# Kernel optimization log

Hardware: AMD Instinct MI355X
Metric: run time of the kernel (lower is better)

The kernel has to match this reference:

```python
import jax, jax.numpy as jnp
import numpy as np

PATCH = 14
LEVELS = 6
DIM = 512
MULT = 4
ITERS = 12
TOKEN_ATTEND_SELF_VALUE = -0.0005


def _grouped_ff(x, w1, b1, w2, b2):
    # x: [b, n, g, d]; per-group 1x1 conv == per-level MLP
    h = jnp.einsum('bnld,lmd->bnlm', x, w1) + b1  # [b,n,g,d*mult]
    h = jax.nn.gelu(h, approximate=False)
    return jnp.einsum('bnlm,ldm->bnld', h, w2) + b2


def _consensus(levels):
    # levels: [b, n, l, d]
    d = levels.shape[-1]
    n = levels.shape[1]
    k = levels / jnp.maximum(jnp.linalg.norm(levels, axis=-1, keepdims=True), 1e-12)
    sim = jnp.einsum('bild,bjld->blij', levels, k) * (d ** -0.5)
    self_mask = jnp.eye(n, dtype=bool)[None, None]  # attend_self=False
    sim = jnp.where(self_mask, TOKEN_ATTEND_SELF_VALUE, sim)
    attn = jax.nn.softmax(sim, axis=-1)
    return jnp.einsum('blij,bjld->bild', attn, levels)


def setup_inputs() -> dict:
    key = jax.random.key(0)
    ks = jax.random.split(key, 12)
    b, c, hw = 16, 1, 224
    pd = PATCH * PATCH * c  # 196
    nps = hw // PATCH
    n = nps * nps  # 256
    s = 0.02
    return {
        'img': jax.random.normal(ks[0], (b, c, hw, hw), jnp.float32),
        'to_tokens_w': jax.random.normal(ks[1], (pd, DIM), jnp.float32) * s,
        'to_tokens_b': jnp.zeros((DIM,), jnp.float32),
        'pos_emb': jax.random.normal(ks[2], (n, DIM), jnp.float32) * s,
        'init_levels': jax.random.normal(ks[3], (LEVELS, DIM), jnp.float32),
        'bu_w1': jax.random.normal(ks[4], (LEVELS, DIM * MULT, DIM), jnp.float32) * s,
        'bu_b1': jnp.zeros((LEVELS, DIM * MULT), jnp.float32),
        'bu_w2': jax.random.normal(ks[5], (LEVELS, DIM, DIM * MULT), jnp.float32) * s,
        'bu_b2': jnp.zeros((LEVELS, DIM), jnp.float32),
        'td_w1': jax.random.normal(ks[6], (LEVELS - 1, DIM * MULT, DIM), jnp.float32) * s,
        'td_b1': jnp.zeros((LEVELS - 1, DIM * MULT), jnp.float32),
        'td_w2': jax.random.normal(ks[7], (LEVELS - 1, DIM, DIM * MULT), jnp.float32) * s,
        'td_b2': jnp.zeros((LEVELS - 1, DIM), jnp.float32),
    }


def reference(img, to_tokens_w, to_tokens_b, pos_emb, init_levels,
              bu_w1, bu_b1, bu_w2, bu_b2, td_w1, td_b1, td_w2, td_b2):
    b, c, H, W = img.shape
    hp, wp = H // PATCH, W // PATCH
    n = hp * wp
    # b c (hp p1) (wp p2) -> b (hp wp) (p1 p2 c)
    x = img.reshape(b, c, hp, PATCH, wp, PATCH)
    x = x.transpose(0, 2, 4, 3, 5, 1).reshape(b, n, PATCH * PATCH * c)
    tokens = x @ to_tokens_w + to_tokens_b          # [b, n, d]
    pos = pos_emb[None, :, None, :]                 # [1, n, 1, d]
    bottom = tokens[:, :, None, :]                  # [b, n, 1, d]
    levels0 = jnp.broadcast_to(init_levels[None, None], (b, n, LEVELS, DIM))
    contrib = jnp.array([4., 4., 4., 4., 4., 3.], jnp.float32)[None, None, :, None]

    def step(levels, _):
        lwi = jnp.concatenate((bottom, levels), axis=2)         # [b, n, L+1, d]
        bu = _grouped_ff(lwi[:, :, :-1], bu_w1, bu_b1, bu_w2, bu_b2)
        td = _grouped_ff(lwi[:, :, 2:] + pos, td_w1, td_b1, td_w2, td_b2)
        td = jnp.pad(td, ((0, 0), (0, 0), (0, 1), (0, 0)))      # zero pad top level
        cons = _consensus(levels)
        new_levels = (levels + bu + td + cons) / contrib
        return new_levels, None

    levels, _ = jax.lax.scan(step, levels0, None, length=ITERS)
    return levels
```

## Files before the change

### kernel.cpp

```cpp
#include <hip/hip_runtime.h>
#include <hip/hip_bf16.h>
#include <math.h>

typedef unsigned short ushort_t;

#define DEV __device__ __forceinline__

DEV float bf2f(ushort_t u) {
  return __uint_as_float(((unsigned int)u) << 16);
}
DEV ushort_t f2bf(float f) {
  unsigned int x = __float_as_uint(f);
  return (ushort_t)((x + 0x7FFFu + ((x >> 16) & 1u)) >> 16);
}

DEV float gelu_f(float x) {
  float z = fabsf(x) * 0.70710678118654752f;
  float t = __builtin_amdgcn_rcpf(1.0f + 0.3275911f * z);
  float p = t * (0.254829592f +
            t * (-0.284496736f +
            t * (1.421413741f +
            t * (-1.453152027f +
            t * 1.061405429f))));
  float e = 1.0f - p * __expf(-z * z);
  float s = (x >= 0.f) ? e : -e;
  return 0.5f * x * (1.0f + s);
}

using bf16x8 = __attribute__((ext_vector_type(8))) __bf16;
using f32x4  = __attribute__((ext_vector_type(4))) float;

DEV void gload16(const ushort_t* g, ushort_t* l) {
  __builtin_amdgcn_global_load_lds((const __attribute__((address_space(1))) void*)g,
                                   (__attribute__((address_space(3))) void*)l, 16, 0, 0);
}

DEV void stage_sw(const ushort_t* g, int ld, ushort_t* lds, int t) {
  int w = t >> 6;
#pragma unroll
  for (int r = 0; r < 4; ++r) {
    int chunk = r * 256 + t;
    int row = chunk >> 3;
    int sw  = ((chunk & 7) ^ (row & 7)) * 8;
    const ushort_t* gp = g + (size_t)row * ld + sw;
    ushort_t* lp = lds + (size_t)(r * 256 + w * 64) * 8;
    gload16(gp, lp);
  }
}

template <typename F>
DEV void gemm_tile(const ushort_t* A, int lda, const ushort_t* B, int ldb, int K, F&& epi) {
  __shared__ alignas(16) ushort_t As[2][128 * 64];
  __shared__ alignas(16) ushort_t Bs[2][128 * 64];
  int t = threadIdx.x;
  int lane = t & 63;
  int w = t >> 6;
  int wr = w >> 1, wc = w & 1;
  const int nk = K >> 6;
  f32x4 acc[4][4];
#pragma unroll
  for (int m = 0; m < 4; ++m)
#pragma unroll
    for (int n = 0; n < 4; ++n) acc[m][n] = (f32x4){0.f, 0.f, 0.f, 0.f};

  int aoff[4][2], boff[4][2];
#pragma unroll
  for (int m = 0; m < 4; ++m)
#pragma unroll
    for (int kk = 0; kk < 2; ++kk) {
      int ks = kk * 4 + (lane >> 4);
      aoff[m][kk] = (wr * 64 + m * 16 + (lane & 15)) * 64 + ((ks ^ (lane & 7)) * 8);
      boff[m][kk] = (wc * 64 + m * 16 + (lane & 15)) * 64 + ((ks ^ (lane & 7)) * 8);
    }

  stage_sw(A, lda, As[0], t);
  stage_sw(B, ldb, Bs[0], t);

  for (int kt = 0; kt < nk; ++kt) {
    int cur = kt & 1;
    int nxt = (kt + 1 < nk) ? kt + 1 : kt;
    stage_sw(A + (size_t)nxt * 64, lda, As[cur ^ 1], t);
    stage_sw(B + (size_t)nxt * 64, ldb, Bs[cur ^ 1], t);
    asm volatile("s_waitcnt vmcnt(8)" ::: "memory");
    __builtin_amdgcn_s_barrier();
    __builtin_amdgcn_sched_barrier(0);
    const ushort_t* asb = &As[cur][0];
    const ushort_t* bsb = &Bs[cur][0];
#pragma unroll
    for (int kk = 0; kk < 2; ++kk) {
      bf16x8 af[4], bfr[4];
#pragma unroll
      for (int m = 0; m < 4; ++m) af[m] = *(const bf16x8*)&asb[aoff[m][kk]];
#pragma unroll
      for (int n = 0; n < 4; ++n) bfr[n] = *(const bf16x8*)&bsb[boff[n][kk]];
      __builtin_amdgcn_s_setprio(1);
#pragma unroll
      for (int m = 0; m < 4; ++m)
#pragma unroll
        for (int n = 0; n < 4; ++n)
          acc[m][n] = __builtin_amdgcn_mfma_f32_16x16x32_bf16(af[m], bfr[n], acc[m][n], 0, 0, 0);
      __builtin_amdgcn_s_setprio(0);
    }
    __builtin_amdgcn_s_barrier();
  }

#pragma unroll
  for (int m = 0; m < 4; ++m)
#pragma unroll
    for (int n = 0; n < 4; ++n)
#pragma unroll
      for (int r = 0; r < 4; ++r) {
        int lr = wr * 64 + m * 16 + (lane >> 4) * 4 + r;
        int lc = wc * 64 + n * 16 + (lane & 15);
        epi(lr, lc, acc[m][n][r]);
      }
}

#define MFMA_QUAD(QM, QN)                                                      \
  _Pragma("unroll") for (int m_ = 0; m_ < 4; ++m_)                             \
  _Pragma("unroll") for (int n_ = 0; n_ < 2; ++n_)                             \
  _Pragma("unroll") for (int kk_ = 0; kk_ < 2; ++kk_)                          \
    acc[QM][QN][m_][n_] = __builtin_amdgcn_mfma_f32_16x16x32_bf16(             \
        aF[m_][kk_], bF[QN][n_][kk_], acc[QM][QN][m_][n_], 0, 0, 0);

template <typename F>
DEV void gemm256(const ushort_t* A, int lda, const ushort_t* B, int ldb, int K, F&& epi) {
  __shared__ alignas(16) ushort_t As[2][256 * 64];
  __shared__ alignas(16) ushort_t Bs[2][256 * 64];
  const int tid = threadIdx.x;
  const int lane = tid & 63;
  const int w = tid >> 6;
  const int ur = w >> 2, uc = w & 3;
  const int nk = K >> 6;

  const int c0 = tid, c1 = 512 + tid;
  const int row0 = c0 >> 3, row1 = c1 >> 3;
  const int sw0 = ((c0 & 7) ^ (row0 & 7)) * 8;
  const int sw1 = ((c1 & 7) ^ (row1 & 7)) * 8;
  const ushort_t* Ab0 = A + (size_t)row0 * lda + sw0;
  const ushort_t* Ab1 = A + (size_t)row1 * lda + sw1;
  const ushort_t* Bb0 = B + (size_t)row0 * ldb + sw0;
  const ushort_t* Bb1 = B + (size_t)row1 * ldb + sw1;
  const int ld0 = (0 * 512 + w * 64) * 8;
  const int ld1 = (1 * 512 + w * 64) * 8;

  auto stageA = [&](int t, int hh, int b) {
    const ushort_t* g0 = Ab0 + (size_t)hh * 128 * lda + t * 64;
    const ushort_t* g1 = Ab1 + (size_t)hh * 128 * lda + t * 64;
    ushort_t* l = &As[b][hh * 8192];
    gload16(g0, l + ld0);
    gload16(g1, l + ld1);
  };
  auto stageB = [&](int t, int hh, int b) {
    const ushort_t* g0 = Bb0 + (size_t)hh * 128 * ldb + t * 64;
    const ushort_t* g1 = Bb1 + (size_t)hh * 128 * ldb + t * 64;
    ushort_t* l = &Bs[b][hh * 8192];
    gload16(g0, l + ld0);
    gload16(g1, l + ld1);
  };

  int aoff[4][2], boff[2][2];
#pragma unroll
  for (int m = 0; m < 4; ++m)
#pragma unroll
    for (int kk = 0; kk < 2; ++kk) {
      int row = ur * 64 + m * 16 + (lane & 15);
      int ks = kk * 4 + (lane >> 4);
      aoff[m][kk] = row * 64 + ((ks ^ (lane & 7)) * 8);
    }
#pragma unroll
  for (int n = 0; n < 2; ++n)
#pragma unroll
    for (int kk = 0; kk < 2; ++kk) {
      int row = uc * 32 + n * 16 + (lane & 15);
      int ks = kk * 4 + (lane >> 4);
      boff[n][kk] = row * 64 + ((ks ^ (lane & 7)) * 8);
    }

  f32x4 acc[2][2][4][2];
#pragma unroll
  for (int qm = 0; qm < 2; ++qm)
#pragma unroll
    for (int qn = 0; qn < 2; ++qn)
#pragma unroll
      for (int m = 0; m < 4; ++m)
#pragma unroll
        for (int n = 0; n < 2; ++n) acc[qm][qn][m][n] = (f32x4){0.f, 0.f, 0.f, 0.f};

  stageA(0, 0, 0);
  stageB(0, 0, 0);
  stageB(0, 1, 0);
  stageA(0, 1, 0);
  stageA(1, 0, 1);
  stageB(1, 0, 1);
  asm volatile("s_waitcnt vmcnt(8)" ::: "memory");
  __builtin_amdgcn_s_barrier();

  bf16x8 aF[4][2], bF[2][2][2];

  for (int t = 0; t < nk; ++t) {
    const int b = t & 1;
    const ushort_t* asb = &As[b][0];
    const ushort_t* bsb = &Bs[b][0];
    const int t1 = (t + 1 < nk) ? t + 1 : nk - 1;
    const int t2 = (t + 2 < nk) ? t + 2 : nk - 1;

#pragma unroll
    for (int m = 0; m < 4; ++m)
#pragma unroll
      for (int kk = 0; kk < 2; ++kk) aF[m][kk] = *(const bf16x8*)&asb[aoff[m][kk]];
#pragma unroll
    for (int n = 0; n < 2; ++n)
#pragma unroll
      for (int kk = 0; kk < 2; ++kk) bF[0][n][kk] = *(const bf16x8*)&bsb[boff[n][kk]];
    stageB(t1, 1, (t + 1) & 1);
    __builtin_amdgcn_s_barrier();
    asm volatile("s_waitcnt lgkmcnt(0)" ::: "memory");
    __builtin_amdgcn_s_setprio(1);
    MFMA_QUAD(0, 0)
    __builtin_amdgcn_s_setprio(0);
    asm volatile("s_waitcnt vmcnt(8)" ::: "memory");
    __builtin_amdgcn_s_barrier();

#pragma unroll
    for (int n = 0; n < 2; ++n)
#pragma unroll
      for (int kk = 0; kk < 2; ++kk) bF[1][n][kk] = *(const bf16x8*)&bsb[boff[n][kk] + 8192];
    stageA(t1, 1, (t + 1) & 1);
    __builtin_amdgcn_s_barrier();
    asm volatile("s_waitcnt lgkmcnt(0)" ::: "memory");
    __builtin_amdgcn_s_setprio(1);
    MFMA_QUAD(0, 1)
    __builtin_amdgcn_s_setprio(0);
    asm volatile("s_waitcnt vmcnt(8)" ::: "memory");
    __builtin_amdgcn_s_barrier();

#pragma unroll
    for (int m = 0; m < 4; ++m)
#pragma unroll
      for (int kk = 0; kk < 2; ++kk) aF[m][kk] = *(const bf16x8*)&asb[aoff[m][kk] + 8192];
    stageA(t2, 0, b);
    __builtin_amdgcn_s_barrier();
    asm volatile("s_waitcnt lgkmcnt(0)" ::: "memory");
    __builtin_amdgcn_s_setprio(1);
    MFMA_QUAD(1, 0)
    __builtin_amdgcn_s_setprio(0);
    __builtin_amdgcn_s_barrier();

    stageB(t2, 0, b);
    __builtin_amdgcn_s_barrier();
    __builtin_amdgcn_s_setprio(1);
    MFMA_QUAD(1, 1)
    __builtin_amdgcn_s_setprio(0);
    asm volatile("s_waitcnt vmcnt(8)" ::: "memory");
    __builtin_amdgcn_s_barrier();
  }
  asm volatile("s_waitcnt vmcnt(0)" ::: "memory");

#pragma unroll
  for (int qm = 0; qm < 2; ++qm)
#pragma unroll
    for (int qn = 0; qn < 2; ++qn)
#pragma unroll
      for (int m = 0; m < 4; ++m)
#pragma unroll
        for (int n = 0; n < 2; ++n)
#pragma unroll
          for (int r = 0; r < 4; ++r) {
            int lr = qm * 128 + ur * 64 + m * 16 + (lane >> 4) * 4 + r;
            int lc = qn * 128 + uc * 32 + n * 16 + (lane & 15);
            epi(lr, lc, acc[qm][qn][m][n][r]);
          }
}

__global__ __launch_bounds__(256) void ff1_kernel(
    int g0, const ushort_t* tokens, const ushort_t* levels_bf, const ushort_t* levels_pos,
    const ushort_t* w1_bf, const float* bu_b1, const float* td_b1, ushort_t* h) {
  int g = g0 + blockIdx.z;
  int tm = blockIdx.x, tn = blockIdx.y;
  const ushort_t* A; int lda;
  if (g == 0)      { A = tokens     + (size_t)tm * 128 * 512;                              lda = 512;  }
  else if (g < 6)  { A = levels_bf  + (size_t)tm * 128 * 3072 + (size_t)(g - 1) * 512;     lda = 3072; }
  else             { A = levels_pos + (size_t)tm * 128 * 2560 + (size_t)(g - 6) * 512;     lda = 2560; }
  const ushort_t* W = w1_bf + (size_t)g * 2048 * 512 + (size_t)tn * 128 * 512;
  const float* bias = (g < 6) ? (bu_b1 + (size_t)g * 2048) : (td_b1 + (size_t)(g - 6) * 2048);
  ushort_t* out = h + ((size_t)(g - g0) * 4096 + (size_t)tm * 128) * 2048 + (size_t)tn * 128;
  gemm_tile(A, lda, W, 512, 512, [&](int lr, int lc, float v) {
    float x = v + bias[tn * 128 + lc];
    out[(size_t)lr * 2048 + lc] = f2bf(gelu_f(x));
  });
}

__global__ __launch_bounds__(512, 2) void ff2_kernel(
    int g0, const ushort_t* h, const ushort_t* w2_bf, const float* bu_b2, const float* td_b2,
    float* levels) {
  int g = g0 + blockIdx.z;
  int tm = blockIdx.x, tn = blockIdx.y;
  const ushort_t* A = h + ((size_t)(g - g0) * 4096 + (size_t)tm * 256) * 2048;
  const ushort_t* W = w2_bf + (size_t)g * 512 * 2048 + (size_t)tn * 256 * 2048;
  int l = (g < 6) ? g : (g - 6);
  const float* bias = (g < 6) ? (bu_b2 + (size_t)g * 512) : (td_b2 + (size_t)(g - 6) * 512);
  gemm256(A, 2048, W, 2048, 2048, [&](int lr, int lc, float v) {
    int bn = tm * 256 + lr;
    int d  = tn * 256 + lc;
    size_t idx = ((size_t)bn * 6 + l) * 512 + d;
    levels[idx] += v + bias[d];
  });
}

__global__ __launch_bounds__(256) void sim_kernel(const ushort_t* levels_bf, const float* invn,
                                                  ushort_t* simattn) {
  int bl = blockIdx.z; int tm = blockIdx.x, tn = blockIdx.y;
  int b = bl / 6, l = bl % 6;
  const ushort_t* A = levels_bf + ((size_t)(b * 256 + tm * 128) * 6 + l) * 512;
  const ushort_t* B = levels_bf + ((size_t)(b * 256 + tn * 128) * 6 + l) * 512;
  const float* inv = invn + (size_t)bl * 256;
  ushort_t* out = simattn + ((size_t)bl * 256 + tm * 128) * 256 + (size_t)tn * 128;
  gemm_tile(A, 3072, B, 3072, 512, [&](int lr, int lc, float v) {
    int i = tm * 128 + lr, j = tn * 128 + lc;
    float s = (i == j) ? -0.0005f : v * inv[j] * 0.044194173824159216f;
    out[(size_t)lr * 256 + lc] = f2bf(s);
  });
}

__global__ __launch_bounds__(256) void softmax_kernel(ushort_t* simattn) {
  int row = blockIdx.x, t = threadIdx.x;
  __shared__ float red[256];
  float x = bf2f(simattn[(size_t)row * 256 + t]);
  red[t] = x;
  __syncthreads();
  for (int s = 128; s > 0; s >>= 1) { if (t < s) red[t] = fmaxf(red[t], red[t + s]); __syncthreads(); }
  float mx = red[0];
  __syncthreads();
  float e = __expf(x - mx);
  red[t] = e;
  __syncthreads();
  for (int s = 128; s > 0; s >>= 1) { if (t < s) red[t] += red[t + s]; __syncthreads(); }
  float den = red[0];
  simattn[(size_t)row * 256 + t] = f2bf(e / den);
}

__global__ __launch_bounds__(256) void pv_kernel(const ushort_t* attn, const ushort_t* levelsT,
                                                 float* levels) {
  int bl = blockIdx.z; int tm = blockIdx.x, tn = blockIdx.y;
  int b = bl / 6, l = bl % 6;
  const ushort_t* A = attn + (size_t)bl * 256 * 256 + (size_t)tm * 128 * 256;
  const ushort_t* B = levelsT + ((size_t)bl * 512 + (size_t)tn * 128) * 256;
  gemm_tile(A, 256, B, 256, 256, [&](int lr, int lc, float v) {
    int n = tm * 128 + lr;
    int d = tn * 128 + lc;
    size_t idx = (((size_t)b * 256 + n) * 6 + l) * 512 + d;
    levels[idx] += v;
  });
}

__global__ __launch_bounds__(128) void prep_kernel(float* levels, const float* pos_emb,
                                                   ushort_t* levels_bf, ushort_t* levels_pos,
                                                   float* invn, int apply) {
  int bid = blockIdx.x;
  int l = bid % 6;
  int bn = bid / 6;
  int n = bn & 255, b = bn >> 8;
  int t = threadIdx.x;
  float4 lv = *(const float4*)&levels[(size_t)bid * 512 + t * 4];
  if (apply) {
    float rc = (l == 5) ? (1.0f / 3.0f) : 0.25f;
    lv.x *= rc; lv.y *= rc; lv.z *= rc; lv.w *= rc;
    *(float4*)&levels[(size_t)bid * 512 + t * 4] = lv;
  }
  float ss = lv.x * lv.x + lv.y * lv.y + lv.z * lv.z + lv.w * lv.w;
#pragma unroll
  for (int off = 32; off > 0; off >>= 1) ss += __shfl_down(ss, off);
  __shared__ float s2[2];
  if ((t & 63) == 0) s2[t >> 6] = ss;
  __syncthreads();
  if (t == 0) {
    float tot = s2[0] + s2[1];
    invn[(size_t)(b * 6 + l) * 256 + n] = 1.0f / fmaxf(sqrtf(tot), 1e-12f);
  }
  ushort4 o;
  o.x = f2bf(lv.x); o.y = f2bf(lv.y); o.z = f2bf(lv.z); o.w = f2bf(lv.w);
  *(ushort4*)&levels_bf[(size_t)bid * 512 + t * 4] = o;
  if (l >= 1) {
    float4 pu = *(const float4*)&pos_emb[(size_t)n * 512 + t * 4];
    ushort4 op;
    op.x = f2bf(lv.x + pu.x);
    op.y = f2bf(lv.y + pu.y);
    op.z = f2bf(lv.z + pu.z);
    op.w = f2bf(lv.w + pu.w);
    *(ushort4*)&levels_pos[((size_t)bn * 5 + (l - 1)) * 512 + t * 4] = op;
  }
}

__global__ __launch_bounds__(256) void transpose_kernel(const float* levels, ushort_t* levelsT) {
  int bl = blockIdx.z; int b = bl / 6, l = bl % 6;
  int n0 = blockIdx.y * 64, d0 = blockIdx.x * 64;
  __shared__ ushort_t tile[64][72];
  int t = threadIdx.x;
#pragma unroll
  for (int rr = 0; rr < 2; ++rr) {
    int c = t + rr * 256;
    int r = c >> 3, c8 = (c & 7) * 8;
    const float* src = &levels[(((size_t)(b * 256 + n0 + r)) * 6 + l) * 512 + d0 + c8];
    float4 v0 = *(const float4*)src;
    float4 v1 = *(const float4*)(src + 4);
    tile[r][c8 + 0] = f2bf(v0.x); tile[r][c8 + 1] = f2bf(v0.y);
    tile[r][c8 + 2] = f2bf(v0.z); tile[r][c8 + 3] = f2bf(v0.w);
    tile[r][c8 + 4] = f2bf(v1.x); tile[r][c8 + 5] = f2bf(v1.y);
    tile[r][c8 + 6] = f2bf(v1.z); tile[r][c8 + 7] = f2bf(v1.w);
  }
  __syncthreads();
#pragma unroll
  for (int rr = 0; rr < 2; ++rr) {
    int c = t + rr * 256;
    int dr = c >> 3, n8 = (c & 7) * 8;
    ushort4 o0, o1;
    o0.x = tile[n8 + 0][dr]; o0.y = tile[n8 + 1][dr]; o0.z = tile[n8 + 2][dr]; o0.w = tile[n8 + 3][dr];
    o1.x = tile[n8 + 4][dr]; o1.y = tile[n8 + 5][dr]; o1.z = tile[n8 + 6][dr]; o1.w = tile[n8 + 7][dr];
    ushort_t* dst = &levelsT[((size_t)bl * 512 + d0 + dr) * 256 + n0 + n8];
    *(ushort4*)dst = o0;
    *(ushort4*)(dst + 4) = o1;
  }
}

__global__ __launch_bounds__(256) void tokens_kernel(const float* img, const float* ttw,
                                                     const float* ttb, ushort_t* tokens) {
  int token = blockIdx.x;
  int b = token >> 8, n = token & 255;
  int ph = n >> 4, pw = n & 15;
  __shared__ float patch[196];
  int t = threadIdx.x;
  if (t < 196) {
    int r = t / 14, cc = t % 14;
    patch[t] = img[(size_t)b * 50176 + (size_t)(ph * 14 + r) * 224 + pw * 14 + cc];
  }
  __syncthreads();
  float a0 = ttb[t];
  float a1 = ttb[t + 256];
  for (int k = 0; k < 196; ++k) {
    float p = patch[k];
    a0 += p * ttw[(size_t)k * 512 + t];
    a1 += p * ttw[(size_t)k * 512 + t + 256];
  }
  tokens[(size_t)token * 512 + t]       = f2bf(a0);
  tokens[(size_t)token * 512 + t + 256] = f2bf(a1);
}

__global__ void init_kernel(const float* init_levels, float* levels) {
  size_t i4 = (size_t)blockIdx.x * 256 + threadIdx.x;
  size_t e0 = i4 * 4;
  int idx = (int)(e0 % 3072);
  *(float4*)&levels[e0] = *(const float4*)&init_levels[idx];
}

__global__ void scale_kernel(float* levels) {
  size_t i4 = (size_t)blockIdx.x * 256 + threadIdx.x;
  size_t e0 = i4 * 4;
  int l = (int)((e0 >> 9) % 6);
  float rc = (l == 5) ? (1.0f / 3.0f) : 0.25f;
  float4 a = *(const float4*)&levels[e0];
  float4 o = {a.x * rc, a.y * rc, a.z * rc, a.w * rc};
  *(float4*)&levels[e0] = o;
}

__global__ void cvt_kernel(const float* src, ushort_t* dst, int n4) {
  int i = blockIdx.x * 256 + threadIdx.x;
  if (i >= n4) return;
  float4 v = ((const float4*)src)[i];
  ushort4 o;
  o.x = f2bf(v.x); o.y = f2bf(v.y); o.z = f2bf(v.z); o.w = f2bf(v.w);
  ((ushort4*)dst)[i] = o;
}

extern "C" void kernel_launch(void* const* d_in, const int* in_sizes, int n_in,
                              void* d_out, int out_size, void* d_ws, size_t ws_size,
                              hipStream_t stream) {
  const float* img    = (const float*)d_in[0];
  const float* ttw    = (const float*)d_in[1];
  const float* ttb    = (const float*)d_in[2];
  const float* pos    = (const float*)d_in[3];
  const float* initlv = (const float*)d_in[4];
  const float* bu_w1  = (const float*)d_in[5];
  const float* bu_b1  = (const float*)d_in[6];
  const float* bu_w2  = (const float*)d_in[7];
  const float* bu_b2  = (const float*)d_in[8];
  const float* td_w1  = (const float*)d_in[9];
  const float* td_b1  = (const float*)d_in[10];
  const float* td_w2  = (const float*)d_in[11];
  const float* td_b2  = (const float*)d_in[12];

  float* levels = (float*)d_out;

  const size_t HB = 16777216ull;

  char* p = (char*)d_ws;
  auto alloc = [&](size_t bytes) { char* r = p; p += (bytes + 255) & ~(size_t)255; return r; };
  float*    invn       = (float*)alloc(24576ull * 4);
  ushort_t* tokens     = (ushort_t*)alloc(2097152ull * 2);
  ushort_t* levels_bf  = (ushort_t*)alloc(12582912ull * 2);
  ushort_t* levels_pos = (ushort_t*)alloc(10485760ull * 2);
  ushort_t* levelsT    = (ushort_t*)alloc(12582912ull * 2);
  ushort_t* simattn    = (ushort_t*)alloc(6291456ull * 2);
  ushort_t* w1_bf      = (ushort_t*)alloc(11534336ull * 2);
  ushort_t* w2_bf      = (ushort_t*)alloc(11534336ull * 2);
  size_t used = (size_t)(p - (char*)d_ws);
  if (used + HB > ws_size) return;
  int gpp = (int)((ws_size - used) / HB);
  if (gpp > 6) gpp = 6;
  ushort_t* h = (ushort_t*)alloc((size_t)gpp * HB);

  cvt_kernel<<<6144, 256, 0, stream>>>(bu_w1, w1_bf, 1572864);
  cvt_kernel<<<5120, 256, 0, stream>>>(td_w1, w1_bf + 6291456ull, 1310720);
  cvt_kernel<<<6144, 256, 0, stream>>>(bu_w2, w2_bf, 1572864);
  cvt_kernel<<<5120, 256, 0, stream>>>(td_w2, w2_bf + 6291456ull, 1310720);
  tokens_kernel<<<4096, 256, 0, stream>>>(img, ttw, ttb, tokens);
  init_kernel<<<12288, 256, 0, stream>>>(initlv, levels);

  for (int it = 0; it < 12; ++it) {
    prep_kernel<<<24576, 128, 0, stream>>>(levels, pos, levels_bf, levels_pos, invn,
                                           it > 0 ? 1 : 0);
    transpose_kernel<<<dim3(8, 4, 96), 256, 0, stream>>>(levels, levelsT);
    sim_kernel<<<dim3(2, 2, 96), 256, 0, stream>>>(levels_bf, invn, simattn);
    softmax_kernel<<<24576, 256, 0, stream>>>(simattn);
    pv_kernel<<<dim3(2, 4, 96), 256, 0, stream>>>(simattn, levelsT, levels);
    for (int g0 = 0; g0 < 11; g0 += gpp) {
      int gn = 11 - g0 < gpp ? 11 - g0 : gpp;
      ff1_kernel<<<dim3(32, 16, gn), 256, 0, stream>>>(g0, tokens, levels_bf, levels_pos,
                                                       w1_bf, bu_b1, td_b1, h);
      ff2_kernel<<<dim3(16, 2, gn), 512, 0, stream>>>(g0, h, w2_bf, bu_b2, td_b2, levels);
    }
  }
  scale_kernel<<<12288, 256, 0, stream>>>(levels);
}
```

Measured before the change: 5.595 ms.

## Permute W1 rows so the FF1 epilogue writes packed bf16 pairs

The first-layer weights are converted to bf16 with a row permutation inside each 32-row block. After this, the two MFMA output tiles a lane holds cover adjacent hidden columns, so the GELU epilogue can store two bf16 values as one 32-bit write instead of scattered 16-bit writes. FF1 also moves to a new, simpler GEMM routine: a single LDS buffer, no XOR swizzle, and a whole accumulator array handed to the epilogue. That trades the old double-buffered, bank-conflict-avoiding staging for the cheaper stores, so it risks LDS bank conflicts and lost load/compute overlap.

```diff
diff --git a/kernel.cpp b/kernel.cpp
--- a/kernel.cpp
+++ b/kernel.cpp
@@ -35,6 +35,17 @@
                                    (__attribute__((address_space(3))) void*)l, 16, 0, 0);
 }
 
+DEV void stage_tile(const ushort_t* g, int ld, ushort_t* lds, int t) {
+  int w = t >> 6;
+#pragma unroll
+  for (int r = 0; r < 4; ++r) {
+    int chunk = r * 256 + t;
+    const ushort_t* gp = g + (size_t)(chunk >> 3) * ld + (size_t)(chunk & 7) * 8;
+    ushort_t* lp = lds + (size_t)(r * 256 + w * 64) * 8;
+    gload16(gp, lp);
+  }
+}
+
 DEV void stage_sw(const ushort_t* g, int ld, ushort_t* lds, int t) {
   int w = t >> 6;
 #pragma unroll
@@ -46,6 +57,45 @@
     ushort_t* lp = lds + (size_t)(r * 256 + w * 64) * 8;
     gload16(gp, lp);
   }
+}
+
+template <typename F>
+DEV void gemm_tileP(const ushort_t* A, int lda, const ushort_t* B, int ldb, int K, F&& epi) {
+  __shared__ alignas(16) ushort_t As[128 * 64];
+  __shared__ alignas(16) ushort_t Bs[128 * 64];
+  int t = threadIdx.x;
+  int lane = t & 63;
+  int w = t >> 6;
+  int wr = w >> 1, wc = w & 1;
+  f32x4 acc[4][4];
+#pragma unroll
+  for (int m = 0; m < 4; ++m)
+#pragma unroll
+    for (int n = 0; n < 4; ++n) acc[m][n] = (f32x4){0.f, 0.f, 0.f, 0.f};
+
+  for (int kt = 0; kt < K; kt += 64) {
+    __syncthreads();
+    stage_tile(A + kt, lda, As, t);
+    stage_tile(B + kt, ldb, Bs, t);
+    __syncthreads();
+#pragma unroll
+    for (int kk = 0; kk < 2; ++kk) {
+      int kb = kk * 32 + (lane >> 4) * 8;
+      bf16x8 af[4], bfr[4];
+#pragma unroll
+      for (int m = 0; m < 4; ++m)
+        af[m] = *(const bf16x8*)&As[(size_t)(wr * 64 + m * 16 + (lane & 15)) * 64 + kb];
+#pragma unroll
+      for (int n = 0; n < 4; ++n)
+        bfr[n] = *(const bf16x8*)&Bs[(size_t)(wc * 64 + n * 16 + (lane & 15)) * 64 + kb];
+#pragma unroll
+      for (int m = 0; m < 4; ++m)
+#pragma unroll
+        for (int n = 0; n < 4; ++n)
+          acc[m][n] = __builtin_amdgcn_mfma_f32_16x16x32_bf16(af[m], bfr[n], acc[m][n], 0, 0, 0);
+    }
+  }
+  epi(wr, wc, lane, acc);
 }
 
 template <typename F>
@@ -285,9 +335,23 @@
   const ushort_t* W = w1_bf + (size_t)g * 2048 * 512 + (size_t)tn * 128 * 512;
   const float* bias = (g < 6) ? (bu_b1 + (size_t)g * 2048) : (td_b1 + (size_t)(g - 6) * 2048);
   ushort_t* out = h + ((size_t)(g - g0) * 4096 + (size_t)tm * 128) * 2048 + (size_t)tn * 128;
-  gemm_tile(A, lda, W, 512, 512, [&](int lr, int lc, float v) {
-    float x = v + bias[tn * 128 + lc];
-    out[(size_t)lr * 2048 + lc] = f2bf(gelu_f(x));
+  gemm_tileP(A, lda, W, 512, 512, [&](int wr, int wc, int lane, f32x4 (&acc)[4][4]) {
+#pragma unroll
+    for (int m = 0; m < 4; ++m)
+#pragma unroll
+      for (int q = 0; q < 2; ++q) {
+        int col = wc * 64 + q * 32 + 2 * (lane & 15);
+        float b0 = bias[tn * 128 + col];
+        float b1 = bias[tn * 128 + col + 1];
+#pragma unroll
+        for (int r = 0; r < 4; ++r) {
+          int lr = wr * 64 + m * 16 + (lane >> 4) * 4 + r;
+          float x0 = gelu_f(acc[m][2 * q][r] + b0);
+          float x1 = gelu_f(acc[m][2 * q + 1][r] + b1);
+          unsigned int pk = (unsigned int)f2bf(x0) | ((unsigned int)f2bf(x1) << 16);
+          *(unsigned int*)&out[(size_t)lr * 2048 + col] = pk;
+        }
+      }
   });
 }
 
@@ -470,6 +534,18 @@
   ushort4 o;
   o.x = f2bf(v.x); o.y = f2bf(v.y); o.z = f2bf(v.z); o.w = f2bf(v.w);
   ((ushort4*)dst)[i] = o;
+}
+
+__global__ void cvt_w1_kernel(const float* src, ushort_t* dst, int nrows) {
+  int i = blockIdx.x * 256 + threadIdx.x;
+  if (i >= nrows * 128) return;
+  int row = i >> 7, k4 = (i & 127) * 4;
+  int grp = row >> 11, rr = row & 2047;
+  int p = (rr & ~31) | ((rr & 1) << 4) | ((rr & 31) >> 1);
+  float4 v = *(const float4*)&src[(size_t)row * 512 + k4];
+  ushort4 o;
+  o.x = f2bf(v.x); o.y = f2bf(v.y); o.z = f2bf(v.z); o.w = f2bf(v.w);
+  *(ushort4*)&dst[((size_t)(grp << 11) + p) * 512 + k4] = o;
 }
 
 extern "C" void kernel_launch(void* const* d_in, const int* in_sizes, int n_in,
@@ -509,8 +585,8 @@
   if (gpp > 6) gpp = 6;
   ushort_t* h = (ushort_t*)alloc((size_t)gpp * HB);
 
-  cvt_kernel<<<6144, 256, 0, stream>>>(bu_w1, w1_bf, 1572864);
-  cvt_kernel<<<5120, 256, 0, stream>>>(td_w1, w1_bf + 6291456ull, 1310720);
+  cvt_w1_kernel<<<6144, 256, 0, stream>>>(bu_w1, w1_bf, 12288);
+  cvt_w1_kernel<<<5120, 256, 0, stream>>>(td_w1, w1_bf + 6291456ull, 10240);
   cvt_kernel<<<6144, 256, 0, stream>>>(bu_w2, w2_bf, 1572864);
   cvt_kernel<<<5120, 256, 0, stream>>>(td_w2, w2_bf + 6291456ull, 1310720);
   tokens_kernel<<<4096, 256, 0, stream>>>(img, ttw, ttb, tokens);
```

Result: faster. 5.383 ms (-3.8%).
